# Performance work log

Hardware: AMD Instinct MI355X
Metric: run time of the kernel (lower is better)

## Reference

```python
import jax, jax.numpy as jnp
import numpy as np

B, T, C, H = 2, 2048, 1024, 16
D = C // H
CURV = 1.0  # clamp_curvature(1.0) -> 1.0
EPS = 1e-5


def layer_norm(x, w, b):
    mu = jnp.mean(x, axis=-1, keepdims=True)
    var = jnp.var(x, axis=-1, keepdims=True)
    return (x - mu) * jax.lax.rsqrt(var + EPS) * w + b


def mobius_addition(x, y, c):
    xn2 = jnp.sum(x * x, axis=-1, keepdims=True)
    yn2 = jnp.sum(y * y, axis=-1, keepdims=True)
    ip = jnp.sum(x * y, axis=-1, keepdims=True)
    num = (1 + 2 * c * ip + c * yn2) * x + (1 - c * xn2) * y
    den = 1 + 2 * c * ip + (c ** 2) * xn2 * yn2
    return num / den


def scaling_factor(x, c):
    xn2 = jnp.sum(x * x, axis=-1, keepdims=True)
    return 2.0 / (1.0 + c * xn2)


def expmap(x, v, c):
    lam = scaling_factor(x, c)
    vn = jnp.linalg.norm(v, axis=-1, keepdims=True)
    second = (1.0 / c ** 0.5) * jnp.tanh(jnp.sqrt(c * lam * vn ** 2 / 2.0)) * v / vn
    return mobius_addition(x, second, c)


def logmap(x, u, c):
    lam = scaling_factor(x, c)
    m = mobius_addition(-x, u, c)
    mn = jnp.linalg.norm(m, axis=-1, keepdims=True)
    cf = 2.0 / (lam * c ** 0.5)
    arg = jnp.clip(jnp.sqrt(c * mn), -0.999, 0.999)
    return cf * jnp.arctanh(arg) * m / mn


def calc_reference_point(x):
    # shift-right by one token, zero at position 0
    return jnp.pad(x[:, :-1, :], ((0, 0), (1, 0), (0, 0)))


def causal_attention(q, k, v):
    # q,k,v: [B,H,T,D]
    scores = jnp.einsum('bhqd,bhkd->bhqk', q, k) / np.sqrt(D).astype(np.float32)
    mask = jnp.tril(jnp.ones((T, T), dtype=bool))
    scores = jnp.where(mask, scores, -jnp.inf)
    att = jax.nn.softmax(scores, axis=-1)
    return jnp.einsum('bhqk,bhkd->bhqd', att, v)


def setup_inputs() -> dict:
    key = jax.random.key(0)
    ks = jax.random.split(key, 6)
    s = 0.02
    return {
        'x': jax.random.normal(ks[0], (B, T, C), jnp.float32),
        'ln1_w': jnp.ones((C,), jnp.float32),
        'ln1_b': jnp.zeros((C,), jnp.float32),
        'W_attn': jax.random.normal(ks[1], (C, 3 * C), jnp.float32) * s,
        'b_attn': jnp.zeros((3 * C,), jnp.float32),
        'W_aproj': jax.random.normal(ks[2], (C, C), jnp.float32) * s,
        'b_aproj': jnp.zeros((C,), jnp.float32),
        'ln2_w': jnp.ones((C,), jnp.float32),
        'ln2_b': jnp.zeros((C,), jnp.float32),
        'W_fc': jax.random.normal(ks[3], (C, 4 * C), jnp.float32) * s,
        'b_fc': jnp.zeros((4 * C,), jnp.float32),
        'W_mproj': jax.random.normal(ks[4], (4 * C, C), jnp.float32) * s,
        'b_mproj': jnp.zeros((C,), jnp.float32),
    }


def reference(x, ln1_w, ln1_b, W_attn, b_attn, W_aproj, b_aproj,
              ln2_w, ln2_b, W_fc, b_fc, W_mproj, b_mproj):
    c = CURV
    # --- attention branch ---
    xn = layer_norm(x, ln1_w, ln1_b)
    ref = calc_reference_point(xn)
    xt = logmap(ref, xn, c)
    qkv = xt @ W_attn + b_attn
    q, k, v = jnp.split(qkv, 3, axis=-1)
    q = q.reshape(B, T, H, D).transpose(0, 2, 1, 3)
    k = k.reshape(B, T, H, D).transpose(0, 2, 1, 3)
    v = v.reshape(B, T, H, D).transpose(0, 2, 1, 3)
    y = causal_attention(q, k, v)
    y = y.transpose(0, 2, 1, 3).reshape(B, T, C)
    y = expmap(ref, y, c)  # map_back_after_attention=True
    y = y @ W_aproj + b_aproj
    x = x + y
    # --- MLP branch (no expmap since map_back_after_attention) ---
    h = layer_norm(x, ln2_w, ln2_b)
    h = jax.nn.gelu(h @ W_fc + b_fc, approximate=False)
    h = h @ W_mproj + b_mproj
    return x + h
```

## Files before the change

kernel.cpp:

```cpp
#include <hip/hip_runtime.h>
#include <hip/hip_bf16.h>
#include <math.h>

#define BDIM 2
#define TSEQ 2048
#define CDIM 1024
#define HNUM 16
#define NROW (BDIM*TSEQ)
#define AST 72

typedef __attribute__((ext_vector_type(8))) short bf16x8_t;
typedef __attribute__((ext_vector_type(4))) float f32x4_t;

__device__ inline float bf2f(__hip_bfloat16 h) { return __bfloat162float(h); }

__device__ inline void unpack8(uint4 u, float* f) {
  unsigned v[4] = {u.x, u.y, u.z, u.w};
  #pragma unroll
  for (int i = 0; i < 4; ++i) {
    union { unsigned u2; float f2; } a, b;
    a.u2 = v[i] << 16;
    b.u2 = v[i] & 0xffff0000u;
    f[2*i]   = a.f2;
    f[2*i+1] = b.f2;
  }
}

__device__ inline void gload16(const void* g, void* l) {
  __builtin_amdgcn_global_load_lds(
      (const __attribute__((address_space(1))) void*)g,
      (__attribute__((address_space(3))) void*)l, 16, 0, 0);
}

template<int N> __device__ inline void waitcnt_vm() {
  asm volatile("s_waitcnt vmcnt(%0)" :: "i"(N) : "memory");
}

__global__ __launch_bounds__(256) void zero32_kernel(float* p, int n) {
  int i = blockIdx.x * 256 + threadIdx.x;
  if (i < n) p[i] = 0.f;
}

__device__ inline void convT_body(const float* __restrict__ src,
    __hip_bfloat16* __restrict__ dst, int K, int N, int bx, int by)
{
  __shared__ float tile[32][33];
  const int k0 = bx * 32, n0 = by * 32;
  const int tr  = threadIdx.x >> 3;
  const int tc4 = (threadIdx.x & 7) * 4;
  float4 v = *(const float4*)(src + (size_t)(k0 + tr) * N + n0 + tc4);
  tile[tr][tc4+0] = v.x; tile[tr][tc4+1] = v.y;
  tile[tr][tc4+2] = v.z; tile[tr][tc4+3] = v.w;
  __syncthreads();
  union { ushort4 u; __hip_bfloat16 h[4]; } o;
  #pragma unroll
  for (int j = 0; j < 4; ++j) o.h[j] = __float2bfloat16(tile[tc4+j][tr]);
  *(ushort4*)(dst + (size_t)(n0 + tr) * K + k0 + tc4) = o.u;
}

__global__ __launch_bounds__(256) void convT_kernel(const float* __restrict__ src,
    __hip_bfloat16* __restrict__ dst, int K, int N)
{
  convT_body(src, dst, K, N, blockIdx.x, blockIdx.y);
}

__global__ __launch_bounds__(256) void convT2_kernel(const float* __restrict__ s1,
    __hip_bfloat16* __restrict__ d1, const float* __restrict__ s2,
    __hip_bfloat16* __restrict__ d2)
{
  int g = blockIdx.x;
  if (g < 4096) {
    convT_body(s1, d1, 1024, 4096, g & 31, g >> 5);
  } else {
    g -= 4096;
    convT_body(s2, d2, 4096, 1024, g & 127, g >> 7);
  }
}

__device__ inline void blk_reduce3(float& a, float& b, float& c, float* red) {
  const int lane = threadIdx.x & 63, wv = threadIdx.x >> 6;
  #pragma unroll
  for (int off = 32; off; off >>= 1) {
    a += __shfl_xor(a, off); b += __shfl_xor(b, off); c += __shfl_xor(c, off);
  }
  if (lane == 0) { red[wv] = a; red[4+wv] = b; red[8+wv] = c; }
  __syncthreads();
  a = red[0]+red[1]+red[2]+red[3];
  b = red[4]+red[5]+red[6]+red[7];
  c = red[8]+red[9]+red[10]+red[11];
}

__global__ __launch_bounds__(256) void ln_kernel(const float* __restrict__ x,
    const float* __restrict__ w, const float* __restrict__ b,
    __hip_bfloat16* __restrict__ out)
{
  const int row = blockIdx.x;
  const size_t base = (size_t)row * CDIM;
  const int lane = threadIdx.x & 63, wv = threadIdx.x >> 6;
  float v[4]; float s = 0.f, s2 = 0.f;
  #pragma unroll
  for (int k = 0; k < 4; ++k) {
    int d = threadIdx.x + k*256;
    float xe = x[base + d];
    v[k] = xe; s += xe; s2 += xe*xe;
  }
  __shared__ float red[8];
  #pragma unroll
  for (int off = 32; off; off >>= 1) { s += __shfl_xor(s, off); s2 += __shfl_xor(s2, off); }
  if (lane == 0) { red[wv] = s; red[4+wv] = s2; }
  __syncthreads();
  s  = red[0]+red[1]+red[2]+red[3];
  s2 = red[4]+red[5]+red[6]+red[7];
  float mu = s * (1.0f/CDIM);
  float var = s2 * (1.0f/CDIM) - mu*mu;
  float rstd = rsqrtf(fmaxf(var, 0.f) + 1e-5f);
  #pragma unroll
  for (int k = 0; k < 4; ++k) {
    int d = threadIdx.x + k*256;
    out[base + d] = __float2bfloat16((v[k]-mu)*rstd*w[d] + b[d]);
  }
}

__global__ __launch_bounds__(256) void scalmix1_kernel(const __hip_bfloat16* __restrict__ xn,
                                                       __hip_bfloat16* __restrict__ xt)
{
  const int row = blockIdx.x;
  const bool has = (row & (TSEQ-1)) != 0;
  const __hip_bfloat16* u  = xn + (size_t)row * CDIM;
  const __hip_bfloat16* xp = xn + (size_t)(has ? row-1 : row) * CDIM;
  float ue[4], xe[4];
  float sxx = 0.f, suu = 0.f, sxu = 0.f;
  #pragma unroll
  for (int k = 0; k < 4; ++k) {
    int d = threadIdx.x + k*256;
    ue[k] = bf2f(u[d]);
    xe[k] = has ? bf2f(xp[d]) : 0.f;
    sxx += xe[k]*xe[k]; suu += ue[k]*ue[k]; sxu += xe[k]*ue[k];
  }
  __shared__ float red[12];
  blk_reduce3(sxx, suu, sxu, red);
  float den = 1.f - 2.f*sxu + sxx*suu;
  float inv = 1.f / fmaxf(den, 1e-30f);
  float cb = 1.f - sxx;
  float ca = 1.f - 2.f*sxu + suu;
  float mm = inv*inv*(cb*cb*suu - 2.f*ca*cb*sxu + ca*ca*sxx);
  float mn = sqrtf(fmaxf(mm, 0.f));
  float arg = fminf(sqrtf(mn), 0.999f);
  float fac = (1.f + sxx) * atanhf(arg) / fmaxf(mn, 1e-30f);
  float P = fac*cb*inv;
  float Q = has ? -fac*ca*inv : 0.f;
  #pragma unroll
  for (int k = 0; k < 4; ++k) {
    int d = threadIdx.x + k*256;
    xt[(size_t)row*CDIM + d] = __float2bfloat16(P*ue[k] + Q*xe[k]);
  }
}

__device__ inline const __hip_bfloat16* slot_ptrc(const __hip_bfloat16* p0,
                                                  const __hip_bfloat16* p1, int s) {
  return (s < 2048) ? p0 + (size_t)s*4096 : p1 + (size_t)(s-2048)*4096;
}
__device__ inline __hip_bfloat16* slot_ptr(__hip_bfloat16* p0, __hip_bfloat16* p1, int s) {
  return (s < 2048) ? p0 + (size_t)s*4096 : p1 + (size_t)(s-2048)*4096;
}

__global__ __launch_bounds__(256) void scalmix2_kernel(const __hip_bfloat16* __restrict__ xn,
    const __hip_bfloat16* __restrict__ y,
    const __hip_bfloat16* __restrict__ pO0, const __hip_bfloat16* __restrict__ pO1,
    const float2* __restrict__ ml,
    __hip_bfloat16* __restrict__ e)
{
  const int row = blockIdx.x;
  const int b = row >> 11, t = row & 2047;
  const int qt = t >> 6, q = t & 63;
  const bool has = (t != 0);
  const __hip_bfloat16* xp = xn + (size_t)(has ? row-1 : row) * CDIM;
  float ve[4], xe[4];

  if (qt < 8) {
    const __hip_bfloat16* vr = y + (size_t)row * CDIM;
    #pragma unroll
    for (int k = 0; k < 4; ++k) ve[k] = bf2f(vr[threadIdx.x + k*256]);
  } else {
    const int nch = (qt >= 24) ? 4 : (qt >= 16) ? 3 : 2;
    const int off = (qt >= 24) ? 40 + (qt-24)*4 : (qt >= 16) ? 16 + (qt-16)*3 : (qt-8)*2;
    #pragma unroll
    for (int k = 0; k < 4; ++k) {
      int d = threadIdx.x + k*256;
      int h = d >> 6, dd = d & 63;
      int s0 = (b*16 + h)*72 + off;
      float mi[4], li[4], M = -1e30f;
      #pragma unroll
      for (int i = 0; i < 4; ++i) if (i < nch) {
        float2 tt = ml[(size_t)(s0+i)*64 + q];
        mi[i] = tt.x; li[i] = tt.y; M = fmaxf(M, tt.x);
      }
      int base = (q>>4)*1024 + (dd>>4)*256 + (q&3)*64 + ((q>>2)&3)*16 + (dd&15);
      float denom = 0.f, acc = 0.f;
      #pragma unroll
      for (int i = 0; i < 4; ++i) if (i < nch) {
        float w = __expf(mi[i] - M);
        denom += li[i]*w;
        acc += w * bf2f(slot_ptrc(pO0, pO1, s0+i)[base]);
      }
      ve[k] = acc / denom;
    }
  }

  float sxx = 0.f, svv = 0.f, sxv = 0.f;
  #pragma unroll
  for (int k = 0; k < 4; ++k) {
    int d = threadIdx.x + k*256;
    xe[k] = has ? bf2f(xp[d]) : 0.f;
    sxx += xe[k]*xe[k]; svv += ve[k]*ve[k]; sxv += xe[k]*ve[k];
  }
  __shared__ float red[12];
  blk_reduce3(sxx, svv, sxv, red);
  float lam = 2.f / (1.f + sxx);
  float vn  = sqrtf(fmaxf(svv, 1e-30f));
  float th  = tanhf(vn * sqrtf(0.5f*lam));
  float s   = th / vn;
  float yn2 = th*th;
  float ip  = s * sxv;
  float den = 1.f + 2.f*ip + sxx*yn2;
  float inv = 1.f / fmaxf(den, 1e-30f);
  float S = (1.f - sxx)*s*inv;
  float R = has ? (1.f + 2.f*ip + yn2)*inv : 0.f;
  #pragma unroll
  for (int k = 0; k < 4; ++k) {
    int d = threadIdx.x + k*256;
    e[(size_t)row*CDIM + d] = __float2bfloat16(S*ve[k] + R*xe[k]);
  }
}

template<int BM, int BN, int MODE>
__global__ __launch_bounds__(256) void gemmT_kernel(
    const __hip_bfloat16* __restrict__ A, int lda,
    const __hip_bfloat16* __restrict__ Bt, int ldb,
    const float* __restrict__ bias,
    const float* __restrict__ res,
    void* __restrict__ outp,
    int N, int K)
{
  __shared__ __align__(16) __hip_bfloat16 As[3][BM*32];
  __shared__ __align__(16) __hip_bfloat16 Bs[3][BN*32];
  const int bm = blockIdx.x, bn = blockIdx.y;
  const int tid = threadIdx.x, lane = tid & 63, wv = tid >> 6;
  constexpr int FM = BM/32, FN = BN/32;
  const int wm = (wv >> 1) * (BM/2), wn = (wv & 1) * (BN/2);
  f32x4_t acc[FM][FN];
  #pragma unroll
  for (int m = 0; m < FM; ++m)
    #pragma unroll
    for (int n = 0; n < FN; ++n) acc[m][n] = (f32x4_t){0.f,0.f,0.f,0.f};

  const int fr = lane & 15, quad = lane >> 4, q8 = quad * 8;
  const int srow = lane >> 2, scol = (lane & 3) * 8;
  constexpr int SA = BM/16, SB = BN/16;
  constexpr int L = SA/4 + SB/4;
  const __hip_bfloat16* Ag = A  + (size_t)(bm*BM + srow)*lda + scol;
  const __hip_bfloat16* Bg = Bt + (size_t)(bn*BN + srow)*ldb + scol;

  const int nk = K/32;

  #pragma unroll
  for (int i = 0; i < SA/4; ++i) {
    int s = wv*(SA/4) + i;
    gload16(Ag + (size_t)(s*16)*lda, &As[0][s*512]);
  }
  #pragma unroll
  for (int i = 0; i < SB/4; ++i) {
    int s = wv*(SB/4) + i;
    gload16(Bg + (size_t)(s*16)*ldb, &Bs[0][s*512]);
  }
  #pragma unroll
  for (int i = 0; i < SA/4; ++i) {
    int s = wv*(SA/4) + i;
    gload16(Ag + (size_t)(s*16)*lda + 32, &As[1][s*512]);
  }
  #pragma unroll
  for (int i = 0; i < SB/4; ++i) {
    int s = wv*(SB/4) + i;
    gload16(Bg + (size_t)(s*16)*ldb + 32, &Bs[1][s*512]);
  }

  int b0 = 0, b1 = 1, b2 = 2;
  for (int t = 0; t < nk; ++t) {
    if (t + 1 < nk) waitcnt_vm<L>(); else waitcnt_vm<0>();
    __builtin_amdgcn_s_barrier();
    __builtin_amdgcn_sched_barrier(0);
    if (t + 2 < nk) {
      const int k0 = (t+2)*32;
      #pragma unroll
      for (int i = 0; i < SA/4; ++i) {
        int s = wv*(SA/4) + i;
        gload16(Ag + (size_t)(s*16)*lda + k0, &As[b2][s*512]);
      }
      #pragma unroll
      for (int i = 0; i < SB/4; ++i) {
        int s = wv*(SB/4) + i;
        gload16(Bg + (size_t)(s*16)*ldb + k0, &Bs[b2][s*512]);
      }
    }
    bf16x8_t af[FM], bfr[FN];
    #pragma unroll
    for (int m = 0; m < FM; ++m) af[m]  = *(const bf16x8_t*)&As[b0][(wm + m*16 + fr)*32 + q8];
    #pragma unroll
    for (int n = 0; n < FN; ++n) bfr[n] = *(const bf16x8_t*)&Bs[b0][(wn + n*16 + fr)*32 + q8];
    __builtin_amdgcn_s_setprio(1);
    #pragma unroll
    for (int m = 0; m < FM; ++m)
      #pragma unroll
      for (int n = 0; n < FN; ++n)
        acc[m][n] = __builtin_amdgcn_mfma_f32_16x16x32_bf16(af[m], bfr[n], acc[m][n], 0, 0, 0);
    __builtin_amdgcn_s_setprio(0);
    int tmp = b0; b0 = b1; b1 = b2; b2 = tmp;
  }

  #pragma unroll
  for (int m = 0; m < FM; ++m)
  #pragma unroll
  for (int n = 0; n < FN; ++n)
  #pragma unroll
  for (int r = 0; r < 4; ++r) {
    int row = bm*BM + wm + m*16 + quad*4 + r;
    int col = bn*BN + wn + n*16 + fr;
    size_t idx = (size_t)row * N + col;
    float v = acc[m][n][r];
    if (MODE == 0) {
      v += bias[col];
      ((__hip_bfloat16*)outp)[idx] = __float2bfloat16(v);
    } else if (MODE == 1) {
      v += bias[col] + res[idx];
      ((float*)outp)[idx] = v;
    } else if (MODE == 2) {
      v += bias[col];
      v = 0.5f * v * (1.0f + erff(v * 0.70710678118654752f));
      ((__hip_bfloat16*)outp)[idx] = __float2bfloat16(v);
    } else {
      v += res[idx];
      ((float*)outp)[idx] = v;
    }
  }
}

__global__ __launch_bounds__(256) void attn_kernel(const __hip_bfloat16* __restrict__ qkv,
                                                   __hip_bfloat16* __restrict__ y,
                                                   __hip_bfloat16* __restrict__ pO0,
                                                   __hip_bfloat16* __restrict__ pO1,
                                                   float2* __restrict__ ml)
{
  const int wid = blockIdx.x;
  int qt, ci;
  if (wid < 32)      { qt = 31 - (wid >> 2); ci = wid & 3; }
  else if (wid < 56) { int w = wid - 32; qt = 23 - w/3; ci = w - (23 - qt)*3; }
  else if (wid < 72) { int w = wid - 56; qt = 15 - (w >> 1); ci = w & 1; }
  else               { qt = 79 - wid; ci = 0; }
  const int tb = ci * 8;
  const int te = min(tb + 8, qt + 1);
  const bool direct = (qt < 8);

  const int pair = blockIdx.y;
  const int b  = pair >> 4;
  const int h  = pair & 15;
  const int tid = threadIdx.x;
  const int lane = tid & 63;
  const int wv = tid >> 6;
  const int t0 = qt * 64;

  __shared__ __align__(16) __hip_bfloat16 Ks[64*AST];
  __shared__ __align__(16) __hip_bfloat16 Vt[64*AST];
  __shared__ __align__(16) __hip_bfloat16 Ps[4][16*AST];

  const int colq = lane & 15, quad = lane >> 4;
  const int q8 = quad * 8;

  const __hip_bfloat16* qp = qkv + ((size_t)(b*TSEQ + t0 + wv*16 + colq))*(3*CDIM) + h*64;
  const bf16x8_t qa0 = *(const bf16x8_t*)(qp + q8);
  const bf16x8_t qa1 = *(const bf16x8_t*)(qp + 32 + q8);

  f32x4_t oacc[4];
  #pragma unroll
  for (int tn = 0; tn < 4; ++tn) oacc[tn] = (f32x4_t){0.f,0.f,0.f,0.f};
  float mr[4] = {-1e30f,-1e30f,-1e30f,-1e30f};
  float lr[4] = {0.f,0.f,0.f,0.f};

  const int jr = tid >> 2;
  const int sg = (tid & 3) * 16;
  const size_t kvbase = ((size_t)(b*TSEQ))*(3*CDIM) + h*64;

  uint4 ck0, ck1, cv0, cv1;
  {
    const __hip_bfloat16* kp = qkv + kvbase + (size_t)(tb*64 + jr)*(3*CDIM) + CDIM + sg;
    ck0 = *(const uint4*)(kp);
    ck1 = *(const uint4*)(kp + 8);
    cv0 = *(const uint4*)(kp + CDIM);
    cv1 = *(const uint4*)(kp + CDIM + 8);
  }
  uint4 nk0 = ck0, nk1 = ck1, nv0 = cv0, nv1 = cv1;

  for (int t = tb; t < te; ++t) {
    __syncthreads();
    {
      *(uint4*)(&Ks[jr*AST + sg])     = ck0;
      *(uint4*)(&Ks[jr*AST + sg + 8]) = ck1;
      union { uint4 u; __hip_bfloat16 hh[8]; } a0, a1;
      a0.u = cv0; a1.u = cv1;
      #pragma unroll
      for (int e = 0; e < 8; ++e) Vt[(sg + e)*AST + jr]     = a0.hh[e];
      #pragma unroll
      for (int e = 0; e < 8; ++e) Vt[(sg + 8 + e)*AST + jr] = a1.hh[e];
    }
    if (t + 1 < te) {
      const __hip_bfloat16* kp = qkv + kvbase + (size_t)((t+1)*64 + jr)*(3*CDIM) + CDIM + sg;
      nk0 = *(const uint4*)(kp);
      nk1 = *(const uint4*)(kp + 8);
      nv0 = *(const uint4*)(kp + CDIM);
      nv1 = *(const uint4*)(kp + CDIM + 8);
    }
    __syncthreads();

    f32x4_t sacc[4];
    __builtin_amdgcn_s_setprio(1);
    #pragma unroll
    for (int tn = 0; tn < 4; ++tn) {
      sacc[tn] = (f32x4_t){0.f,0.f,0.f,0.f};
      bf16x8_t bk0 = *(const bf16x8_t*)(&Ks[(tn*16 + colq)*AST + q8]);
      sacc[tn] = __builtin_amdgcn_mfma_f32_16x16x32_bf16(qa0, bk0, sacc[tn], 0, 0, 0);
      bf16x8_t bk1 = *(const bf16x8_t*)(&Ks[(tn*16 + colq)*AST + 32 + q8]);
      sacc[tn] = __builtin_amdgcn_mfma_f32_16x16x32_bf16(qa1, bk1, sacc[tn], 0, 0, 0);
    }
    __builtin_amdgcn_s_setprio(0);

    float sc[4][4];
    #pragma unroll
    for (int tn = 0; tn < 4; ++tn)
    #pragma unroll
    for (int r = 0; r < 4; ++r) sc[tn][r] = sacc[tn][r] * 0.125f;
    if (t == qt) {
      #pragma unroll
      for (int tn = 0; tn < 4; ++tn)
      #pragma unroll
      for (int r = 0; r < 4; ++r) {
        int key = t*64 + tn*16 + colq;
        int row = t0 + wv*16 + quad*4 + r;
        if (key > row) sc[tn][r] = -1e30f;
      }
    }

    float psum[4] = {0.f,0.f,0.f,0.f};
    #pragma unroll
    for (int tn = 0; tn < 4; ++tn)
    #pragma unroll
    for (int r = 0; r < 4; ++r) {
      float p = __expf(sc[tn][r] - mr[r]);
      psum[r] += p;
      Ps[wv][(quad*4 + r)*AST + tn*16 + colq] = __float2bfloat16(p);
    }
    #pragma unroll
    for (int r = 0; r < 4; ++r) {
      #pragma unroll
      for (int off = 8; off; off >>= 1) psum[r] += __shfl_xor(psum[r], off);
    }
    bool trig = !(psum[0] <= 1e5f) || !(psum[1] <= 1e5f) ||
                !(psum[2] <= 1e5f) || !(psum[3] <= 1e5f);
    if (__any(trig)) {
      float mx[4];
      #pragma unroll
      for (int r = 0; r < 4; ++r) {
        mx[r] = fmaxf(fmaxf(sc[0][r], sc[1][r]), fmaxf(sc[2][r], sc[3][r]));
        #pragma unroll
        for (int off = 8; off; off >>= 1) mx[r] = fmaxf(mx[r], __shfl_xor(mx[r], off));
      }
      #pragma unroll
      for (int r = 0; r < 4; ++r) {
        float mn = fmaxf(mr[r], mx[r]);
        float al = __expf(mr[r] - mn);
        mr[r] = mn;
        lr[r] *= al;
        #pragma unroll
        for (int tn = 0; tn < 4; ++tn) oacc[tn][r] *= al;
        psum[r] = 0.f;
      }
      #pragma unroll
      for (int tn = 0; tn < 4; ++tn)
      #pragma unroll
      for (int r = 0; r < 4; ++r) {
        float p = __expf(sc[tn][r] - mr[r]);
        psum[r] += p;
        Ps[wv][(quad*4 + r)*AST + tn*16 + colq] = __float2bfloat16(p);
      }
      #pragma unroll
      for (int r = 0; r < 4; ++r) {
        #pragma unroll
        for (int off = 8; off; off >>= 1) psum[r] += __shfl_xor(psum[r], off);
      }
    }
    #pragma unroll
    for (int r = 0; r < 4; ++r) lr[r] += psum[r];

    bf16x8_t pa0 = *(const bf16x8_t*)(&Ps[wv][colq*AST + q8]);
    bf16x8_t pa1 = *(const bf16x8_t*)(&Ps[wv][colq*AST + 32 + q8]);
    __builtin_amdgcn_s_setprio(1);
    #pragma unroll
    for (int tn = 0; tn < 4; ++tn) {
      bf16x8_t vb0 = *(const bf16x8_t*)(&Vt[(tn*16 + colq)*AST + q8]);
      oacc[tn] = __builtin_amdgcn_mfma_f32_16x16x32_bf16(pa0, vb0, oacc[tn], 0, 0, 0);
      bf16x8_t vb1 = *(const bf16x8_t*)(&Vt[(tn*16 + colq)*AST + 32 + q8]);
      oacc[tn] = __builtin_amdgcn_mfma_f32_16x16x32_bf16(pa1, vb1, oacc[tn], 0, 0, 0);
    }
    __builtin_amdgcn_s_setprio(0);

    ck0 = nk0; ck1 = nk1; cv0 = nv0; cv1 = nv1;
  }

  if (direct) {
    __hip_bfloat16* yp = y + ((size_t)(b*TSEQ + t0 + wv*16))*CDIM + h*64;
    #pragma unroll
    for (int tn = 0; tn < 4; ++tn)
    #pragma unroll
    for (int r = 0; r < 4; ++r) {
      yp[(size_t)(quad*4 + r)*CDIM + tn*16 + colq] = __float2bfloat16(oacc[tn][r] / lr[r]);
    }
  } else {
    int off = (qt >= 24) ? 40 + (qt-24)*4 : (qt >= 16) ? 16 + (qt-16)*3 : (qt-8)*2;
    int s = pair*72 + off + ci;
    __hip_bfloat16* op = slot_ptr(pO0, pO1, s);
    #pragma unroll
    for (int tn = 0; tn < 4; ++tn)
    #pragma unroll
    for (int r = 0; r < 4; ++r) {
      op[wv*1024 + tn*256 + r*64 + lane] = __float2bfloat16(oacc[tn][r]);
    }
    if (colq == 0) {
      #pragma unroll
      for (int r = 0; r < 4; ++r)
        ml[(size_t)s*64 + wv*16 + quad*4 + r] = make_float2(mr[r], lr[r]);
    }
  }
}

extern "C" void kernel_launch(void* const* d_in, const int* in_sizes, int n_in,
                              void* d_out, int out_size, void* d_ws, size_t ws_size,
                              hipStream_t stream)
{
  float* out = (float*)d_out;
  __hip_bfloat16* ybuf = (__hip_bfloat16*)d_out;
  float* x2d = (float*)d_out;
  char* ws = (char*)d_ws;
  const size_t KB = 1024, MB = 1024*1024;

  if (ws_size < 49*MB) {
    zero32_kernel<<<(out_size + 255)/256, 256, 0, stream>>>(out, out_size);
    return;
  }

  const float* x      = (const float*)d_in[0];
  const float* ln1w   = (const float*)d_in[1];
  const float* ln1b   = (const float*)d_in[2];
  const float* Wattn  = (const float*)d_in[3];
  const float* battn  = (const float*)d_in[4];
  const float* Waproj = (const float*)d_in[5];
  const float* baproj = (const float*)d_in[6];
  const float* ln2w   = (const float*)d_in[7];
  const float* ln2b   = (const float*)d_in[8];
  const float* Wfc    = (const float*)d_in[9];
  const float* bfc    = (const float*)d_in[10];
  const float* Wmproj = (const float*)d_in[11];
  const float* bmproj = (const float*)d_in[12];

  __hip_bfloat16* xn   = (__hip_bfloat16*)(ws + 64*KB);
  char* big            = ws + 64*KB + 8*MB;
  __hip_bfloat16* qkv  = (__hip_bfloat16*)big;
  __hip_bfloat16* gbuf = (__hip_bfloat16*)big;
  __hip_bfloat16* ebuf = (__hip_bfloat16*)(big + 16*MB);
  __hip_bfloat16* hbuf = xn;
  char* creg           = ws + 64*KB + 32*MB;
  __hip_bfloat16* cWattnT  = (__hip_bfloat16*)creg;
  __hip_bfloat16* xt       = (__hip_bfloat16*)(creg + 8*MB);
  __hip_bfloat16* cWaprojT = (__hip_bfloat16*)creg;
  __hip_bfloat16* cWfcT    = (__hip_bfloat16*)creg;
  __hip_bfloat16* cWmT     = (__hip_bfloat16*)(creg + 8*MB);
  __hip_bfloat16* pO0      = (__hip_bfloat16*)creg;
  __hip_bfloat16* pO1      = (__hip_bfloat16*)((char*)d_out + 8*MB);
  float2* mlbuf            = (float2*)((char*)d_out + 10*MB);

  convT_kernel<<<dim3(32, 96), 256, 0, stream>>>(Wattn,  cWattnT,  1024, 3072);

  ln_kernel<<<NROW, 256, 0, stream>>>(x, ln1w, ln1b, xn);
  scalmix1_kernel<<<NROW, 256, 0, stream>>>(xn, xt);
  gemmT_kernel<128,128,0><<<dim3(32, 24), 256, 0, stream>>>(
      xt, 1024, cWattnT, 1024, battn, nullptr, qkv, 3072, 1024);
  attn_kernel<<<dim3(80, BDIM*HNUM), 256, 0, stream>>>(qkv, ybuf, pO0, pO1, mlbuf);
  scalmix2_kernel<<<NROW, 256, 0, stream>>>(xn, ybuf, pO0, pO1, mlbuf, ebuf);
  convT_kernel<<<dim3(32, 32), 256, 0, stream>>>(Waproj, cWaprojT, 1024, 1024);
  gemmT_kernel<64,64,1><<<dim3(64, 16), 256, 0, stream>>>(
      ebuf, 1024, cWaprojT, 1024, baproj, x, x2d, 1024, 1024);
  convT2_kernel<<<8192, 256, 0, stream>>>(Wfc, cWfcT, Wmproj, cWmT);
  ln_kernel<<<NROW, 256, 0, stream>>>(x2d, ln2w, ln2b, hbuf);
  for (int c = 0; c < 2; ++c) {
    gemmT_kernel<64,128,2><<<dim3(64, 16), 256, 0, stream>>>(
        hbuf, 1024, cWfcT + (size_t)c*2048*1024, 1024, bfc + 2048*c, nullptr, gbuf,
        2048, 1024);
    const __hip_bfloat16* Bc = cWmT + 2048*c;
    if (c == 0) {
      gemmT_kernel<64,64,1><<<dim3(64, 16), 256, 0, stream>>>(
          gbuf, 2048, Bc, 4096, bmproj, x2d, x2d, 1024, 2048);
    } else {
      gemmT_kernel<64,64,7><<<dim3(64, 16), 256, 0, stream>>>(
          gbuf, 2048, Bc, 4096, nullptr, x2d, out, 1024, 2048);
    }
  }
}
```

Baseline: 455.7 us.

## Use 128-row query tiles with 512-thread attention blocks and lazy softmax rescale

The attention kernel now gives each block 128 query rows (8 waves, 512 threads) instead of 64, so every K/V tile loaded into shared memory serves twice as many queries. Split-KV slot bookkeeping, partial-output strides and the combine step in scalmix2 are reindexed to match. The online softmax now computes the row max first and rescales only when it grows by more than 8, replacing the earlier sum-overflow check and its recompute path. The costs are fewer blocks in the grid, which hurts load balance and occupancy, and extra causal masking work on the last two KV tiles.

```diff
diff --git a/kernel.cpp b/kernel.cpp
--- a/kernel.cpp
+++ b/kernel.cpp
@@ -158,10 +158,10 @@
 
 __device__ inline const __hip_bfloat16* slot_ptrc(const __hip_bfloat16* p0,
                                                   const __hip_bfloat16* p1, int s) {
-  return (s < 2048) ? p0 + (size_t)s*4096 : p1 + (size_t)(s-2048)*4096;
+  return (s < 1024) ? p0 + (size_t)s*8192 : p1 + (size_t)(s-1024)*8192;
 }
 __device__ inline __hip_bfloat16* slot_ptr(__hip_bfloat16* p0, __hip_bfloat16* p1, int s) {
-  return (s < 2048) ? p0 + (size_t)s*4096 : p1 + (size_t)(s-2048)*4096;
+  return (s < 1024) ? p0 + (size_t)s*8192 : p1 + (size_t)(s-1024)*8192;
 }
 
 __global__ __launch_bounds__(256) void scalmix2_kernel(const __hip_bfloat16* __restrict__ xn,
@@ -172,27 +172,27 @@
 {
   const int row = blockIdx.x;
   const int b = row >> 11, t = row & 2047;
-  const int qt = t >> 6, q = t & 63;
+  const int qt2 = t >> 7, q = t & 127;
   const bool has = (t != 0);
   const __hip_bfloat16* xp = xn + (size_t)(has ? row-1 : row) * CDIM;
   float ve[4], xe[4];
 
-  if (qt < 8) {
+  if (qt2 < 4) {
     const __hip_bfloat16* vr = y + (size_t)row * CDIM;
     #pragma unroll
     for (int k = 0; k < 4; ++k) ve[k] = bf2f(vr[threadIdx.x + k*256]);
   } else {
-    const int nch = (qt >= 24) ? 4 : (qt >= 16) ? 3 : 2;
-    const int off = (qt >= 24) ? 40 + (qt-24)*4 : (qt >= 16) ? 16 + (qt-16)*3 : (qt-8)*2;
+    const int nch = (qt2 >= 12) ? 4 : (qt2 >= 8) ? 3 : 2;
+    const int off = (qt2 >= 12) ? 20 + (qt2-12)*4 : (qt2 >= 8) ? 8 + (qt2-8)*3 : (qt2-4)*2;
     #pragma unroll
     for (int k = 0; k < 4; ++k) {
       int d = threadIdx.x + k*256;
       int h = d >> 6, dd = d & 63;
-      int s0 = (b*16 + h)*72 + off;
+      int s0 = (b*16 + h)*36 + off;
       float mi[4], li[4], M = -1e30f;
       #pragma unroll
       for (int i = 0; i < 4; ++i) if (i < nch) {
-        float2 tt = ml[(size_t)(s0+i)*64 + q];
+        float2 tt = ml[(size_t)(s0+i)*128 + q];
         mi[i] = tt.x; li[i] = tt.y; M = fmaxf(M, tt.x);
       }
       int base = (q>>4)*1024 + (dd>>4)*256 + (q&3)*64 + ((q>>2)&3)*16 + (dd&15);
@@ -344,21 +344,21 @@
   }
 }
 
-__global__ __launch_bounds__(256) void attn_kernel(const __hip_bfloat16* __restrict__ qkv,
+__global__ __launch_bounds__(512) void attn_kernel(const __hip_bfloat16* __restrict__ qkv,
                                                    __hip_bfloat16* __restrict__ y,
                                                    __hip_bfloat16* __restrict__ pO0,
                                                    __hip_bfloat16* __restrict__ pO1,
                                                    float2* __restrict__ ml)
 {
   const int wid = blockIdx.x;
-  int qt, ci;
-  if (wid < 32)      { qt = 31 - (wid >> 2); ci = wid & 3; }
-  else if (wid < 56) { int w = wid - 32; qt = 23 - w/3; ci = w - (23 - qt)*3; }
-  else if (wid < 72) { int w = wid - 56; qt = 15 - (w >> 1); ci = w & 1; }
-  else               { qt = 79 - wid; ci = 0; }
+  int qt2, ci;
+  if (wid < 16)      { qt2 = 15 - (wid >> 2); ci = wid & 3; }
+  else if (wid < 28) { int w = wid - 16; qt2 = 11 - w/3; ci = w - (11 - qt2)*3; }
+  else if (wid < 36) { int w = wid - 28; qt2 = 7 - (w >> 1); ci = w & 1; }
+  else               { qt2 = 39 - wid; ci = 0; }
   const int tb = ci * 8;
-  const int te = min(tb + 8, qt + 1);
-  const bool direct = (qt < 8);
+  const int te = min(tb + 8, 2*qt2 + 2);
+  const bool direct = (qt2 < 4);
 
   const int pair = blockIdx.y;
   const int b  = pair >> 4;
@@ -366,11 +366,11 @@
   const int tid = threadIdx.x;
   const int lane = tid & 63;
   const int wv = tid >> 6;
-  const int t0 = qt * 64;
+  const int t0 = qt2 * 128;
 
   __shared__ __align__(16) __hip_bfloat16 Ks[64*AST];
   __shared__ __align__(16) __hip_bfloat16 Vt[64*AST];
-  __shared__ __align__(16) __hip_bfloat16 Ps[4][16*AST];
+  __shared__ __align__(16) __hip_bfloat16 Ps[8][16*AST];
 
   const int colq = lane & 15, quad = lane >> 4;
   const int q8 = quad * 8;
@@ -385,38 +385,30 @@
   float mr[4] = {-1e30f,-1e30f,-1e30f,-1e30f};
   float lr[4] = {0.f,0.f,0.f,0.f};
 
-  const int jr = tid >> 2;
-  const int sg = (tid & 3) * 16;
+  const int jr = tid >> 3;
+  const int sg = (tid & 7) * 8;
   const size_t kvbase = ((size_t)(b*TSEQ))*(3*CDIM) + h*64;
 
-  uint4 ck0, ck1, cv0, cv1;
+  uint4 ck, cv;
   {
     const __hip_bfloat16* kp = qkv + kvbase + (size_t)(tb*64 + jr)*(3*CDIM) + CDIM + sg;
-    ck0 = *(const uint4*)(kp);
-    ck1 = *(const uint4*)(kp + 8);
-    cv0 = *(const uint4*)(kp + CDIM);
-    cv1 = *(const uint4*)(kp + CDIM + 8);
-  }
-  uint4 nk0 = ck0, nk1 = ck1, nv0 = cv0, nv1 = cv1;
+    ck = *(const uint4*)(kp);
+    cv = *(const uint4*)(kp + CDIM);
+  }
+  uint4 nk = ck, nv = cv;
 
   for (int t = tb; t < te; ++t) {
     __syncthreads();
     {
-      *(uint4*)(&Ks[jr*AST + sg])     = ck0;
-      *(uint4*)(&Ks[jr*AST + sg + 8]) = ck1;
-      union { uint4 u; __hip_bfloat16 hh[8]; } a0, a1;
-      a0.u = cv0; a1.u = cv1;
-      #pragma unroll
-      for (int e = 0; e < 8; ++e) Vt[(sg + e)*AST + jr]     = a0.hh[e];
-      #pragma unroll
-      for (int e = 0; e < 8; ++e) Vt[(sg + 8 + e)*AST + jr] = a1.hh[e];
+      *(uint4*)(&Ks[jr*AST + sg]) = ck;
+      union { uint4 u; __hip_bfloat16 hh[8]; } a0; a0.u = cv;
+      #pragma unroll
+      for (int e = 0; e < 8; ++e) Vt[(sg + e)*AST + jr] = a0.hh[e];
     }
     if (t + 1 < te) {
       const __hip_bfloat16* kp = qkv + kvbase + (size_t)((t+1)*64 + jr)*(3*CDIM) + CDIM + sg;
-      nk0 = *(const uint4*)(kp);
-      nk1 = *(const uint4*)(kp + 8);
-      nv0 = *(const uint4*)(kp + CDIM);
-      nv1 = *(const uint4*)(kp + CDIM + 8);
+      nk = *(const uint4*)(kp);
+      nv = *(const uint4*)(kp + CDIM);
     }
     __syncthreads();
 
@@ -437,7 +429,7 @@
     for (int tn = 0; tn < 4; ++tn)
     #pragma unroll
     for (int r = 0; r < 4; ++r) sc[tn][r] = sacc[tn][r] * 0.125f;
-    if (t == qt) {
+    if (t >= 2*qt2) {
       #pragma unroll
       for (int tn = 0; tn < 4; ++tn)
       #pragma unroll
@@ -448,30 +440,16 @@
       }
     }
 
-    float psum[4] = {0.f,0.f,0.f,0.f};
-    #pragma unroll
-    for (int tn = 0; tn < 4; ++tn)
+    float mx[4];
     #pragma unroll
     for (int r = 0; r < 4; ++r) {
-      float p = __expf(sc[tn][r] - mr[r]);
-      psum[r] += p;
-      Ps[wv][(quad*4 + r)*AST + tn*16 + colq] = __float2bfloat16(p);
-    }
-    #pragma unroll
-    for (int r = 0; r < 4; ++r) {
-      #pragma unroll
-      for (int off = 8; off; off >>= 1) psum[r] += __shfl_xor(psum[r], off);
-    }
-    bool trig = !(psum[0] <= 1e5f) || !(psum[1] <= 1e5f) ||
-                !(psum[2] <= 1e5f) || !(psum[3] <= 1e5f);
-    if (__any(trig)) {
-      float mx[4];
-      #pragma unroll
-      for (int r = 0; r < 4; ++r) {
-        mx[r] = fmaxf(fmaxf(sc[0][r], sc[1][r]), fmaxf(sc[2][r], sc[3][r]));
-        #pragma unroll
-        for (int off = 8; off; off >>= 1) mx[r] = fmaxf(mx[r], __shfl_xor(mx[r], off));
-      }
+      mx[r] = fmaxf(fmaxf(sc[0][r], sc[1][r]), fmaxf(sc[2][r], sc[3][r]));
+      #pragma unroll
+      for (int off = 8; off; off >>= 1) mx[r] = fmaxf(mx[r], __shfl_xor(mx[r], off));
+    }
+    bool grow = (mx[0] > mr[0] + 8.f) || (mx[1] > mr[1] + 8.f) ||
+                (mx[2] > mr[2] + 8.f) || (mx[3] > mr[3] + 8.f);
+    if (__any(grow)) {
       #pragma unroll
       for (int r = 0; r < 4; ++r) {
         float mn = fmaxf(mr[r], mx[r]);
@@ -480,24 +458,23 @@
         lr[r] *= al;
         #pragma unroll
         for (int tn = 0; tn < 4; ++tn) oacc[tn][r] *= al;
-        psum[r] = 0.f;
       }
-      #pragma unroll
-      for (int tn = 0; tn < 4; ++tn)
-      #pragma unroll
-      for (int r = 0; r < 4; ++r) {
-        float p = __expf(sc[tn][r] - mr[r]);
-        psum[r] += p;
-        Ps[wv][(quad*4 + r)*AST + tn*16 + colq] = __float2bfloat16(p);
-      }
-      #pragma unroll
-      for (int r = 0; r < 4; ++r) {
-        #pragma unroll
-        for (int off = 8; off; off >>= 1) psum[r] += __shfl_xor(psum[r], off);
-      }
-    }
-    #pragma unroll
-    for (int r = 0; r < 4; ++r) lr[r] += psum[r];
+    }
+    float psum[4] = {0.f,0.f,0.f,0.f};
+    #pragma unroll
+    for (int tn = 0; tn < 4; ++tn)
+    #pragma unroll
+    for (int r = 0; r < 4; ++r) {
+      float p = __expf(sc[tn][r] - mr[r]);
+      psum[r] += p;
+      Ps[wv][(quad*4 + r)*AST + tn*16 + colq] = __float2bfloat16(p);
+    }
+    #pragma unroll
+    for (int r = 0; r < 4; ++r) {
+      #pragma unroll
+      for (int off = 8; off; off >>= 1) psum[r] += __shfl_xor(psum[r], off);
+      lr[r] += psum[r];
+    }
 
     bf16x8_t pa0 = *(const bf16x8_t*)(&Ps[wv][colq*AST + q8]);
     bf16x8_t pa1 = *(const bf16x8_t*)(&Ps[wv][colq*AST + 32 + q8]);
@@ -511,7 +488,7 @@
     }
     __builtin_amdgcn_s_setprio(0);
 
-    ck0 = nk0; ck1 = nk1; cv0 = nv0; cv1 = nv1;
+    ck = nk; cv = nv;
   }
 
   if (direct) {
@@ -523,8 +500,8 @@
       yp[(size_t)(quad*4 + r)*CDIM + tn*16 + colq] = __float2bfloat16(oacc[tn][r] / lr[r]);
     }
   } else {
-    int off = (qt >= 24) ? 40 + (qt-24)*4 : (qt >= 16) ? 16 + (qt-16)*3 : (qt-8)*2;
-    int s = pair*72 + off + ci;
+    int off = (qt2 >= 12) ? 20 + (qt2-12)*4 : (qt2 >= 8) ? 8 + (qt2-8)*3 : (qt2-4)*2;
+    int s = pair*36 + off + ci;
     __hip_bfloat16* op = slot_ptr(pO0, pO1, s);
     #pragma unroll
     for (int tn = 0; tn < 4; ++tn)
@@ -535,7 +512,7 @@
     if (colq == 0) {
       #pragma unroll
       for (int r = 0; r < 4; ++r)
-        ml[(size_t)s*64 + wv*16 + quad*4 + r] = make_float2(mr[r], lr[r]);
+        ml[(size_t)s*128 + wv*16 + quad*4 + r] = make_float2(mr[r], lr[r]);
     }
   }
 }
@@ -591,7 +568,7 @@
   scalmix1_kernel<<<NROW, 256, 0, stream>>>(xn, xt);
   gemmT_kernel<128,128,0><<<dim3(32, 24), 256, 0, stream>>>(
       xt, 1024, cWattnT, 1024, battn, nullptr, qkv, 3072, 1024);
-  attn_kernel<<<dim3(80, BDIM*HNUM), 256, 0, stream>>>(qkv, ybuf, pO0, pO1, mlbuf);
+  attn_kernel<<<dim3(40, BDIM*HNUM), 512, 0, stream>>>(qkv, ybuf, pO0, pO1, mlbuf);
   scalmix2_kernel<<<NROW, 256, 0, stream>>>(xn, ybuf, pO0, pO1, mlbuf, ebuf);
   convT_kernel<<<dim3(32, 32), 256, 0, stream>>>(Waproj, cWaprojT, 1024, 1024);
   gemmT_kernel<64,64,1><<<dim3(64, 16), 256, 0, stream>>>(
```

After: 446.8 us. No clear change (-2.0%).
